# Kernel tuning notes

Measured on AMD Instinct MI355X. Metric: run time of the kernel, lower is better.

The kernel has to match this reference:

```python
import jax, jax.numpy as jnp
import numpy as np

H = 16  # num_heads

def _toroidal_bias(S, dtype):
    # float mask: +1.0 at (i, (i-1)%S), (i,i), (i, (i+1)%S); PyTorch ADDS float attn_mask to scores
    eye = jnp.eye(S, dtype=dtype)
    return eye + jnp.roll(eye, 1, axis=1) + jnp.roll(eye, -1, axis=1)

def setup_inputs() -> dict:
    key = jax.random.key(0)
    ks = jax.random.split(key, 7)
    E = 1024
    S, B = 2048, 2
    sc = 0.02
    return {
        "x": jax.random.normal(ks[0], (S, B, E), dtype=jnp.float32),
        "w_tor": jax.random.normal(ks[1], (E, E), dtype=jnp.float32) * sc,
        "b_tor": jax.random.normal(ks[2], (E,), dtype=jnp.float32) * sc,
        "in_proj_w": jax.random.normal(ks[3], (3 * E, E), dtype=jnp.float32) * sc,
        "in_proj_b": jax.random.normal(ks[4], (3 * E,), dtype=jnp.float32) * sc,
        "out_w": jax.random.normal(ks[5], (E, E), dtype=jnp.float32) * sc,
        "out_b": jax.random.normal(ks[6], (E,), dtype=jnp.float32) * sc,
    }

def reference(x, w_tor, b_tor, in_proj_w, in_proj_b, out_w, out_b):
    S, B, E = x.shape
    hd = E // H
    scale = 1.0 / jnp.sqrt(jnp.asarray(hd, dtype=x.dtype))
    # toroidal projection, then fused in_proj (self-attention: q=k=v=x_toroidal)
    xt = x @ w_tor.T + b_tor                      # (S,B,E)
    qkv = xt @ in_proj_w.T + in_proj_b            # (S,B,3E)
    q, k, v = jnp.split(qkv, 3, axis=-1)
    def to_heads(t):
        return t.reshape(S, B, H, hd).transpose(1, 2, 0, 3)  # (B,H,S,hd)
    q, k, v = to_heads(q), to_heads(k), to_heads(v)
    bias = _toroidal_bias(S, x.dtype)             # (S,S) additive float mask
    scores = jnp.einsum('bhqd,bhkd->bhqk', q * scale, k) + bias
    attn = jax.nn.softmax(scores, axis=-1)
    o = jnp.einsum('bhqk,bhkd->bhqd', attn, v)    # (B,H,S,hd)
    o = o.transpose(2, 0, 1, 3).reshape(S, B, E)
    return o @ out_w.T + out_b
```

## Files before the change

### kernel.cpp

```cpp
#include <hip/hip_runtime.h>

#define S_LEN 2048
#define NB    2
#define EMB   1024
#define NH    16
#define HD    64

typedef __bf16 bf16_t;
typedef bf16_t bf16x8 __attribute__((ext_vector_type(8)));
typedef bf16_t bf16x4v __attribute__((ext_vector_type(4)));
typedef float  f32x4  __attribute__((ext_vector_type(4)));

#define L2E 1.44269504f

__device__ __forceinline__ void g2l16(const void* g, void* l) {
    auto gp = reinterpret_cast<const unsigned int __attribute__((address_space(1)))*>(
        reinterpret_cast<uintptr_t>(g));
    auto lp = reinterpret_cast<unsigned int __attribute__((address_space(3)))*>(
        reinterpret_cast<uintptr_t>(l));
    __builtin_amdgcn_global_load_lds(gp, lp, 16, 0, 0);
}

__global__ __launch_bounds__(256) void cast4_f32_bf16(
    const float* __restrict__ s0, bf16_t* __restrict__ d0,
    const float* __restrict__ s1, bf16_t* __restrict__ d1,
    const float* __restrict__ s2, bf16_t* __restrict__ d2,
    const float* __restrict__ s3, bf16_t* __restrict__ d3)
{
    long i = (long)blockIdx.x * 256 + threadIdx.x;
    const float* s; bf16_t* d; long off;
    if (i < 1048576)      { s = s0; d = d0; off = i; }
    else if (i < 1310720) { s = s1; d = d1; off = i - 1048576; }
    else if (i < 2097152) { s = s2; d = d2; off = i - 1310720; }
    else                  { s = s3; d = d3; off = i - 2097152; }
    float4 v = ((const float4*)s)[off];
    bf16x4v o;
    o[0] = (bf16_t)v.x; o[1] = (bf16_t)v.y; o[2] = (bf16_t)v.z; o[3] = (bf16_t)v.w;
    *(bf16x4v*)(d + off * 4) = o;
}

template<int TN, int MODE>
__global__ __launch_bounds__(256) void gemm_bt_bf16(
    const bf16_t* __restrict__ A, const bf16_t* __restrict__ W,
    const float* __restrict__ bias, void* __restrict__ Cout,
    bf16_t* __restrict__ Qp, bf16_t* __restrict__ Kp, bf16_t* __restrict__ Vtp,
    int M, int N, int K)
{
    constexpr int MB = (TN == 128) ? 4 : 2;
    __shared__ __align__(16) bf16_t As[2][128 * 32];
    __shared__ __align__(16) bf16_t Bs[2][TN * 32];

    const int tid  = threadIdx.x;
    const int lane = tid & 63;
    const int w    = tid >> 6;
    const int lm   = lane & 15;
    const int lq   = lane >> 4;
    const long m0  = (long)blockIdx.y * 128;
    const long n0  = (long)blockIdx.x * TN;
    const int wm0  = (TN == 128) ? (w >> 1) * 64 : w * 32;
    const int wn0  = (TN == 128) ? (w & 1) * 64 : 0;

    f32x4 acc[MB][4];
#pragma unroll
    for (int i = 0; i < MB; ++i)
#pragma unroll
        for (int j = 0; j < 4; ++j) acc[i][j] = (f32x4){0.f, 0.f, 0.f, 0.f};

    auto stage = [&](int k0, int buf) {
        bf16_t* asb = &As[buf][0];
        bf16_t* bsb = &Bs[buf][0];
#pragma unroll
        for (int j = 0; j < 2; ++j) {
            int a   = (w * 2 + j) * 64 + lane;
            int row = a >> 2;
            int c   = (a & 3) ^ ((row >> 1) & 3);
            g2l16(A + (m0 + row) * K + k0 + c * 8, asb + (w * 2 + j) * 512);
        }
#pragma unroll
        for (int j = 0; j < TN / 64; ++j) {
            int a   = (w * (TN / 64) + j) * 64 + lane;
            int row = a >> 2;
            int c   = (a & 3) ^ ((row >> 1) & 3);
            g2l16(W + (n0 + row) * K + k0 + c * 8, bsb + (w * (TN / 64) + j) * 512);
        }
    };

    stage(0, 0);
    for (int k0 = 0; k0 < K; k0 += 32) {
        const int cur = (k0 >> 5) & 1;
        asm volatile("s_waitcnt vmcnt(0)" ::: "memory");
        __syncthreads();
        if (k0 + 32 < K) stage(k0 + 32, cur ^ 1);

        bf16x8 af[MB], bfr[4];
#pragma unroll
        for (int mb = 0; mb < MB; ++mb) {
            int r = wm0 + mb * 16 + lm;
            af[mb] = *(const bf16x8*)&As[cur][r * 32 + ((lq ^ ((r >> 1) & 3)) << 3)];
        }
#pragma unroll
        for (int nb = 0; nb < 4; ++nb) {
            int r = wn0 + nb * 16 + lm;
            bfr[nb] = *(const bf16x8*)&Bs[cur][r * 32 + ((lq ^ ((r >> 1) & 3)) << 3)];
        }
#pragma unroll
        for (int mb = 0; mb < MB; ++mb)
#pragma unroll
            for (int nb = 0; nb < 4; ++nb)
                acc[mb][nb] = __builtin_amdgcn_mfma_f32_16x16x32_bf16(
                    af[mb], bfr[nb], acc[mb][nb], 0, 0, 0);
    }

    float b4[4];
#pragma unroll
    for (int nb = 0; nb < 4; ++nb) b4[nb] = bias[n0 + wn0 + nb * 16 + lm];

#pragma unroll
    for (int mb = 0; mb < MB; ++mb) {
#pragma unroll
        for (int r = 0; r < 4; ++r) {
            long m = m0 + wm0 + mb * 16 + lq * 4 + r;
#pragma unroll
            for (int nb = 0; nb < 4; ++nb) {
                int n   = (int)n0 + wn0 + nb * 16 + lm;
                float v = acc[mb][nb][r] + b4[nb];
                if (MODE == 0) {
                    ((float*)Cout)[m * N + n] = v;
                } else if (MODE == 1) {
                    ((bf16_t*)Cout)[m * N + n] = (bf16_t)v;
                } else {
                    int sec  = n >> 10;
                    int nloc = n & 1023;
                    int h    = nloc >> 6;
                    int d    = nloc & 63;
                    int s    = (int)(m >> 1), b = (int)(m & 1);
                    int bh   = b * 16 + h;
                    if (sec == 0) {
                        Qp[((size_t)(bh * S_LEN + s)) * 64 + d] =
                            (bf16_t)(v * (0.125f * L2E));
                    } else if (sec == 1) {
                        Kp[((size_t)(bh * S_LEN + s)) * 64 + d] = (bf16_t)v;
                    } else {
                        int local = s & 63;
                        int pos   = ((local & 15) << 2) | (local >> 4);
                        Vtp[((size_t)(bh * 64 + d)) * S_LEN + (s & ~63) + pos] =
                            (bf16_t)v;
                    }
                }
            }
        }
    }
}

__global__ __launch_bounds__(256) void attn_mfma(
    const bf16_t* __restrict__ Qb, const bf16_t* __restrict__ Kb,
    const bf16_t* __restrict__ Vtb, bf16_t* __restrict__ O)
{
    __shared__ __align__(16) bf16_t Ks[2][64 * 64];
    __shared__ __align__(16) bf16_t Vts[2][64 * 64];
    __shared__ __align__(16) bf16_t Ps[4][16 * 64];

    const int tid  = threadIdx.x;
    const int lane = tid & 63;
    const int w    = tid >> 6;
    const int bh   = blockIdx.x >> 5;
    const int qt   = blockIdx.x & 31;
    const int lm   = lane & 15;
    const int lq   = lane >> 4;
    const int sr   = lane >> 3;
    const int chunk = (lane & 7) ^ (sr & 7);

    const bf16_t* qbase = Qb + ((size_t)bh * S_LEN + qt * 64 + w * 16 + lm) * 64 + lq * 8;
    const bf16x8 qf0 = *(const bf16x8*)(qbase);
    const bf16x8 qf1 = *(const bf16x8*)(qbase + 32);

    f32x4 oacc[4];
#pragma unroll
    for (int i = 0; i < 4; ++i) oacc[i] = (f32x4){0.f, 0.f, 0.f, 0.f};
    float plsum[4] = {0.f, 0.f, 0.f, 0.f};

    bf16_t* psw = &Ps[w][0];

    auto stageKV = [&](int kt, int buf) {
        bf16_t* ksb = &Ks[buf][0];
        bf16_t* vsb = &Vts[buf][0];
        const bf16_t* kt_g = Kb + ((size_t)bh * S_LEN + kt * 64) * 64;
        g2l16(kt_g + (size_t)(w * 16 + sr) * 64 + chunk * 8,     ksb + (w * 16) * 64);
        g2l16(kt_g + (size_t)(w * 16 + 8 + sr) * 64 + chunk * 8, ksb + (w * 16 + 8) * 64);
        const bf16_t* vt_g = Vtb + (size_t)bh * 64 * S_LEN + kt * 64;
        g2l16(vt_g + (size_t)(w * 16 + sr) * S_LEN + chunk * 8,     vsb + (w * 16) * 64);
        g2l16(vt_g + (size_t)(w * 16 + 8 + sr) * S_LEN + chunk * 8, vsb + (w * 16 + 8) * 64);
    };

    stageKV(0, 0);
    for (int kt = 0; kt < 32; ++kt) {
        const int cur = kt & 1;
        asm volatile("s_waitcnt vmcnt(0)" ::: "memory");
        __syncthreads();
        if (kt < 31) stageKV(kt + 1, cur ^ 1);

        f32x4 S[4];
#pragma unroll
        for (int nb = 0; nb < 4; ++nb) {
            int key = nb * 16 + lm;
            bf16x8 kf0 = *(const bf16x8*)&Ks[cur][key * 64 + (((lq)     ^ (key & 7)) << 3)];
            bf16x8 kf1 = *(const bf16x8*)&Ks[cur][key * 64 + (((4 + lq) ^ (key & 7)) << 3)];
            f32x4 z = (f32x4){0.f, 0.f, 0.f, 0.f};
            z = __builtin_amdgcn_mfma_f32_16x16x32_bf16(qf0, kf0, z, 0, 0, 0);
            z = __builtin_amdgcn_mfma_f32_16x16x32_bf16(qf1, kf1, z, 0, 0, 0);
            S[nb] = z;
        }

        int ktd = (kt - qt) & 31;
        if (ktd <= 1 || ktd == 31) {
#pragma unroll
            for (int nb = 0; nb < 4; ++nb) {
                int key = kt * 64 + nb * 16 + lm;
#pragma unroll
                for (int r = 0; r < 4; ++r) {
                    int qrow = qt * 64 + w * 16 + lq * 4 + r;
                    int diff = (key - qrow) & (S_LEN - 1);
                    if (diff <= 1 || diff == S_LEN - 1) S[nb][r] += L2E;
                }
            }
        }

#pragma unroll
        for (int r = 0; r < 4; ++r) {
            int rowp = lq * 4 + r;
            bf16x4v pk;
#pragma unroll
            for (int nb = 0; nb < 4; ++nb) {
                float p = __builtin_amdgcn_exp2f(S[nb][r]);
                plsum[r] += p;
                pk[nb] = (bf16_t)p;
            }
            *(bf16x4v*)&psw[rowp * 64 + (((lm >> 1) ^ (rowp & 7)) << 3) + ((lm & 1) << 2)] = pk;
        }

        bf16x8 pf0 = *(const bf16x8*)&psw[lm * 64 + ((lq       ^ (lm & 7)) << 3)];
        bf16x8 pf1 = *(const bf16x8*)&psw[lm * 64 + (((4 | lq) ^ (lm & 7)) << 3)];

#pragma unroll
        for (int nbd = 0; nbd < 4; ++nbd) {
            int d = nbd * 16 + lm;
            bf16x8 vf0 = *(const bf16x8*)&Vts[cur][d * 64 + (((lq)     ^ (d & 7)) << 3)];
            bf16x8 vf1 = *(const bf16x8*)&Vts[cur][d * 64 + (((4 + lq) ^ (d & 7)) << 3)];
            oacc[nbd] = __builtin_amdgcn_mfma_f32_16x16x32_bf16(pf0, vf0, oacc[nbd], 0, 0, 0);
            oacc[nbd] = __builtin_amdgcn_mfma_f32_16x16x32_bf16(pf1, vf1, oacc[nbd], 0, 0, 0);
        }
    }

#pragma unroll
    for (int off = 1; off < 16; off <<= 1)
#pragma unroll
        for (int r = 0; r < 4; ++r)
            plsum[r] += __shfl_xor(plsum[r], off, 64);

    const int b = bh >> 4, h = bh & 15;
#pragma unroll
    for (int r = 0; r < 4; ++r) {
        float inv = 1.0f / plsum[r];
        int s = qt * 64 + w * 16 + lq * 4 + r;
        size_t rowbase = ((size_t)(s * NB + b)) * EMB + h * 64 + lm;
#pragma unroll
        for (int nbd = 0; nbd < 4; ++nbd)
            O[rowbase + nbd * 16] = (bf16_t)(oacc[nbd][r] * inv);
    }
}

extern "C" void kernel_launch(void* const* d_in, const int* in_sizes, int n_in,
                              void* d_out, int out_size, void* d_ws, size_t ws_size,
                              hipStream_t stream)
{
    const float* x         = (const float*)d_in[0];
    const float* w_tor     = (const float*)d_in[1];
    const float* b_tor     = (const float*)d_in[2];
    const float* in_proj_w = (const float*)d_in[3];
    const float* in_proj_b = (const float*)d_in[4];
    const float* out_w     = (const float*)d_in[5];
    const float* out_b     = (const float*)d_in[6];
    float* out = (float*)d_out;

    const int M = S_LEN * NB;

    char* base = (char*)d_ws;
    bf16_t* xb    = (bf16_t*)(base);
    bf16_t* wtorb = (bf16_t*)(base + ( 8ull << 20));
    bf16_t* ipwb  = (bf16_t*)(base + (10ull << 20));
    bf16_t* outwb = (bf16_t*)(base + (16ull << 20));
    bf16_t* xtb   = (bf16_t*)(base + (18ull << 20));
    bf16_t* Kb    = (bf16_t*)(base + (26ull << 20));
    bf16_t* Vtb   = (bf16_t*)(base + (34ull << 20));
    bf16_t* Qb    = xb;
    bf16_t* Ob    = xtb;

    cast4_f32_bf16<<<dim3(9216), 256, 0, stream>>>(
        x, xb, w_tor, wtorb, in_proj_w, ipwb, out_w, outwb);

    gemm_bt_bf16<64, 1><<<dim3(EMB / 64, M / 128), 256, 0, stream>>>(
        xb, wtorb, b_tor, xtb, nullptr, nullptr, nullptr, M, EMB, EMB);

    gemm_bt_bf16<128, 2><<<dim3(3 * EMB / 128, M / 128), 256, 0, stream>>>(
        xtb, ipwb, in_proj_b, nullptr, Qb, Kb, Vtb, M, 3 * EMB, EMB);

    attn_mfma<<<dim3(32 * 32), 256, 0, stream>>>(Qb, Kb, Vtb, Ob);

    gemm_bt_bf16<64, 0><<<dim3(EMB / 64, M / 128), 256, 0, stream>>>(
        Ob, outwb, out_b, out, nullptr, nullptr, nullptr, M, EMB, EMB);
}
```

Baseline: 226.2 us.

## Restructure attention kernel around 32x32 MFMA with wave-split key and d halves

Rewrites the attention kernel so each wave computes a 32x32 score tile with 32x32x16 MFMAs, splitting keys across wave pairs and output head-dims across the same pairs. K and V fragments are now loaded straight from global memory into registers, replacing the double-buffered LDS staging. Only P goes through a double-buffered LDS tile, with one barrier per iteration, and row sums are combined across waves at the end. The V-transpose epilogue drops its permuted layout, and launch bounds request higher occupancy. The trade is less LDS traffic and synchronisation against more redundant global/L2 reads and exposed load latency without prefetch.

```diff
diff --git a/kernel.cpp b/kernel.cpp
--- a/kernel.cpp
+++ b/kernel.cpp
@@ -10,6 +10,7 @@
 typedef bf16_t bf16x8 __attribute__((ext_vector_type(8)));
 typedef bf16_t bf16x4v __attribute__((ext_vector_type(4)));
 typedef float  f32x4  __attribute__((ext_vector_type(4)));
+typedef float  f32x16 __attribute__((ext_vector_type(16)));
 
 #define L2E 1.44269504f
 
@@ -141,10 +142,7 @@
                     } else if (sec == 1) {
                         Kp[((size_t)(bh * S_LEN + s)) * 64 + d] = (bf16_t)v;
                     } else {
-                        int local = s & 63;
-                        int pos   = ((local & 15) << 2) | (local >> 4);
-                        Vtp[((size_t)(bh * 64 + d)) * S_LEN + (s & ~63) + pos] =
-                            (bf16_t)v;
+                        Vtp[((size_t)(bh * 64 + d)) * S_LEN + s] = (bf16_t)v;
                     }
                 }
             }
@@ -152,120 +150,126 @@
     }
 }
 
-__global__ __launch_bounds__(256) void attn_mfma(
+__global__ __launch_bounds__(256, 4) void attn_mfma(
     const bf16_t* __restrict__ Qb, const bf16_t* __restrict__ Kb,
     const bf16_t* __restrict__ Vtb, bf16_t* __restrict__ O)
 {
-    __shared__ __align__(16) bf16_t Ks[2][64 * 64];
-    __shared__ __align__(16) bf16_t Vts[2][64 * 64];
-    __shared__ __align__(16) bf16_t Ps[4][16 * 64];
+    __shared__ __align__(16) bf16_t Ps[2][64 * 64];
 
     const int tid  = threadIdx.x;
     const int lane = tid & 63;
     const int w    = tid >> 6;
+    const int kh   = w & 1;
+    const int qh   = w >> 1;
     const int bh   = blockIdx.x >> 5;
     const int qt   = blockIdx.x & 31;
-    const int lm   = lane & 15;
-    const int lq   = lane >> 4;
-    const int sr   = lane >> 3;
-    const int chunk = (lane & 7) ^ (sr & 7);
-
-    const bf16_t* qbase = Qb + ((size_t)bh * S_LEN + qt * 64 + w * 16 + lm) * 64 + lq * 8;
-    const bf16x8 qf0 = *(const bf16x8*)(qbase);
-    const bf16x8 qf1 = *(const bf16x8*)(qbase + 32);
-
-    f32x4 oacc[4];
-#pragma unroll
-    for (int i = 0; i < 4; ++i) oacc[i] = (f32x4){0.f, 0.f, 0.f, 0.f};
-    float plsum[4] = {0.f, 0.f, 0.f, 0.f};
-
-    bf16_t* psw = &Ps[w][0];
-
-    auto stageKV = [&](int kt, int buf) {
-        bf16_t* ksb = &Ks[buf][0];
-        bf16_t* vsb = &Vts[buf][0];
-        const bf16_t* kt_g = Kb + ((size_t)bh * S_LEN + kt * 64) * 64;
-        g2l16(kt_g + (size_t)(w * 16 + sr) * 64 + chunk * 8,     ksb + (w * 16) * 64);
-        g2l16(kt_g + (size_t)(w * 16 + 8 + sr) * 64 + chunk * 8, ksb + (w * 16 + 8) * 64);
-        const bf16_t* vt_g = Vtb + (size_t)bh * 64 * S_LEN + kt * 64;
-        g2l16(vt_g + (size_t)(w * 16 + sr) * S_LEN + chunk * 8,     vsb + (w * 16) * 64);
-        g2l16(vt_g + (size_t)(w * 16 + 8 + sr) * S_LEN + chunk * 8, vsb + (w * 16 + 8) * 64);
-    };
-
-    stageKV(0, 0);
+    const int l5   = lane & 31;
+    const int hi   = lane >> 5;
+    const int qm   = l5 & 15;
+
+    const bf16_t* qrow = Qb + ((size_t)bh * S_LEN + qt * 64 + qh * 32 + l5) * 64 + hi * 8;
+    bf16x8 qf[4];
+#pragma unroll
+    for (int ds = 0; ds < 4; ++ds) qf[ds] = *(const bf16x8*)(qrow + ds * 16);
+
+    const bf16_t* kptr = Kb + ((size_t)bh * S_LEN + kh * 32 + l5) * 64 + hi * 8;
+    const bf16_t* vptr = Vtb + ((size_t)bh * 64 + kh * 32 + l5) * S_LEN + hi * 8;
+
+    bf16_t* pw[4];
+#pragma unroll
+    for (int rq = 0; rq < 4; ++rq)
+        pw[rq] = &Ps[0][(qh * 32 + l5) * 64 + (((kh * 8 + 2 * rq + hi) ^ qm) << 2)];
+    const bf16_t* pr[8];
+#pragma unroll
+    for (int ks = 0; ks < 4; ++ks)
+#pragma unroll
+        for (int e = 0; e < 2; ++e)
+            pr[ks * 2 + e] = &Ps[0][(qh * 32 + l5) * 64 + (((ks * 4 + hi * 2 + e) ^ qm) << 2)];
+
+    f32x16 oacc;
+#pragma unroll
+    for (int i = 0; i < 16; ++i) oacc[i] = 0.f;
+    float plsum = 0.f;
+
     for (int kt = 0; kt < 32; ++kt) {
-        const int cur = kt & 1;
-        asm volatile("s_waitcnt vmcnt(0)" ::: "memory");
-        __syncthreads();
-        if (kt < 31) stageKV(kt + 1, cur ^ 1);
-
-        f32x4 S[4];
-#pragma unroll
-        for (int nb = 0; nb < 4; ++nb) {
-            int key = nb * 16 + lm;
-            bf16x8 kf0 = *(const bf16x8*)&Ks[cur][key * 64 + (((lq)     ^ (key & 7)) << 3)];
-            bf16x8 kf1 = *(const bf16x8*)&Ks[cur][key * 64 + (((4 + lq) ^ (key & 7)) << 3)];
-            f32x4 z = (f32x4){0.f, 0.f, 0.f, 0.f};
-            z = __builtin_amdgcn_mfma_f32_16x16x32_bf16(qf0, kf0, z, 0, 0, 0);
-            z = __builtin_amdgcn_mfma_f32_16x16x32_bf16(qf1, kf1, z, 0, 0, 0);
-            S[nb] = z;
-        }
+        const int pofs = (kt & 1) * 4096;
+
+        bf16x8 kf[4];
+#pragma unroll
+        for (int ds = 0; ds < 4; ++ds) kf[ds] = *(const bf16x8*)(kptr + ds * 16);
+
+        f32x16 sacc;
+#pragma unroll
+        for (int i = 0; i < 16; ++i) sacc[i] = 0.f;
+#pragma unroll
+        for (int ds = 0; ds < 4; ++ds)
+            sacc = __builtin_amdgcn_mfma_f32_32x32x16_bf16(kf[ds], qf[ds], sacc, 0, 0, 0);
 
         int ktd = (kt - qt) & 31;
         if (ktd <= 1 || ktd == 31) {
-#pragma unroll
-            for (int nb = 0; nb < 4; ++nb) {
-                int key = kt * 64 + nb * 16 + lm;
-#pragma unroll
-                for (int r = 0; r < 4; ++r) {
-                    int qrow = qt * 64 + w * 16 + lq * 4 + r;
-                    int diff = (key - qrow) & (S_LEN - 1);
-                    if (diff <= 1 || diff == S_LEN - 1) S[nb][r] += L2E;
-                }
+            int qrow_g = qt * 64 + qh * 32 + l5;
+#pragma unroll
+            for (int r = 0; r < 16; ++r) {
+                int key  = kt * 64 + kh * 32 + (r & 3) + 8 * (r >> 2) + 4 * hi;
+                int diff = (key - qrow_g) & (S_LEN - 1);
+                if (diff <= 1 || diff == S_LEN - 1) sacc[r] += L2E;
             }
         }
 
 #pragma unroll
-        for (int r = 0; r < 4; ++r) {
-            int rowp = lq * 4 + r;
+        for (int rq = 0; rq < 4; ++rq) {
             bf16x4v pk;
 #pragma unroll
-            for (int nb = 0; nb < 4; ++nb) {
-                float p = __builtin_amdgcn_exp2f(S[nb][r]);
-                plsum[r] += p;
-                pk[nb] = (bf16_t)p;
+            for (int e2 = 0; e2 < 4; ++e2) {
+                float p = __builtin_amdgcn_exp2f(sacc[rq * 4 + e2]);
+                plsum += p;
+                pk[e2] = (bf16_t)p;
             }
-            *(bf16x4v*)&psw[rowp * 64 + (((lm >> 1) ^ (rowp & 7)) << 3) + ((lm & 1) << 2)] = pk;
-        }
-
-        bf16x8 pf0 = *(const bf16x8*)&psw[lm * 64 + ((lq       ^ (lm & 7)) << 3)];
-        bf16x8 pf1 = *(const bf16x8*)&psw[lm * 64 + (((4 | lq) ^ (lm & 7)) << 3)];
-
-#pragma unroll
-        for (int nbd = 0; nbd < 4; ++nbd) {
-            int d = nbd * 16 + lm;
-            bf16x8 vf0 = *(const bf16x8*)&Vts[cur][d * 64 + (((lq)     ^ (d & 7)) << 3)];
-            bf16x8 vf1 = *(const bf16x8*)&Vts[cur][d * 64 + (((4 + lq) ^ (d & 7)) << 3)];
-            oacc[nbd] = __builtin_amdgcn_mfma_f32_16x16x32_bf16(pf0, vf0, oacc[nbd], 0, 0, 0);
-            oacc[nbd] = __builtin_amdgcn_mfma_f32_16x16x32_bf16(pf1, vf1, oacc[nbd], 0, 0, 0);
-        }
-    }
-
-#pragma unroll
-    for (int off = 1; off < 16; off <<= 1)
-#pragma unroll
-        for (int r = 0; r < 4; ++r)
-            plsum[r] += __shfl_xor(plsum[r], off, 64);
+            *(bf16x4v*)(pw[rq] + pofs) = pk;
+        }
+
+        bf16x8 vf[4];
+#pragma unroll
+        for (int ks = 0; ks < 4; ++ks) vf[ks] = *(const bf16x8*)(vptr + ks * 16);
+
+        __syncthreads();
+
+#pragma unroll
+        for (int ks = 0; ks < 4; ++ks) {
+            bf16x4v lo  = *(const bf16x4v*)(pr[ks * 2 + 0] + pofs);
+            bf16x4v hi4 = *(const bf16x4v*)(pr[ks * 2 + 1] + pofs);
+            bf16x8 pf;
+#pragma unroll
+            for (int j = 0; j < 4; ++j) { pf[j] = lo[j]; pf[4 + j] = hi4[j]; }
+            oacc = __builtin_amdgcn_mfma_f32_32x32x16_bf16(pf, vf[ks], oacc, 0, 0, 0);
+        }
+
+        kptr += 64 * 64;
+        vptr += 64;
+    }
+
+    plsum += __shfl_xor(plsum, 32, 64);
+    __syncthreads();
+    float* Lsum = (float*)&Ps[0][0];
+    if (lane < 32) Lsum[kh * 64 + qh * 32 + lane] = plsum;
+    __syncthreads();
+
+    float inv[4][4];
+#pragma unroll
+    for (int rq = 0; rq < 4; ++rq) {
+        f32x4 a = *(const f32x4*)&Lsum[qh * 32 + 8 * rq + 4 * hi];
+        f32x4 c = *(const f32x4*)&Lsum[64 + qh * 32 + 8 * rq + 4 * hi];
+#pragma unroll
+        for (int e2 = 0; e2 < 4; ++e2) inv[rq][e2] = 1.0f / (a[e2] + c[e2]);
+    }
 
     const int b = bh >> 4, h = bh & 15;
 #pragma unroll
-    for (int r = 0; r < 4; ++r) {
-        float inv = 1.0f / plsum[r];
-        int s = qt * 64 + w * 16 + lq * 4 + r;
-        size_t rowbase = ((size_t)(s * NB + b)) * EMB + h * 64 + lm;
-#pragma unroll
-        for (int nbd = 0; nbd < 4; ++nbd)
-            O[rowbase + nbd * 16] = (bf16_t)(oacc[nbd][r] * inv);
+    for (int r = 0; r < 16; ++r) {
+        int qrel = (r & 3) + 8 * (r >> 2) + 4 * hi;
+        int s = qt * 64 + qh * 32 + qrel;
+        O[((size_t)(s * NB + b)) * EMB + h * 64 + kh * 32 + l5] =
+            (bf16_t)(oacc[r] * inv[r >> 2][r & 3]);
     }
 }
 
```

Measured after the change: 285.3 us. +26.1%, slower.
